# Optimization experiments

Measured on AMD Instinct MI355X. Metric: run time of the kernel, lower is better.

The kernel has to match this reference:

```python
import jax, jax.numpy as jnp
import numpy as np

ANG = 5   # angular resolution (u = v = 5, n = 25 views)
CH = 64   # input channels
D = 2 * CH  # spa_dim + ang_dim + fre_dim = c/2 + c/2 + c = 128
NEG = -1e15


def _l2(x):
    # torch F.normalize over the contraction axis (last axis of folded layout)
    n = jnp.sqrt(jnp.sum(x * x, axis=-1, keepdims=True))
    return x / jnp.maximum(n, 1e-12)


def setup_inputs() -> dict:
    key = jax.random.key(0)
    ks = jax.random.split(key, 8)
    b, c, n, h, w = 4, CH, ANG * ANG, 32, 32
    d = D
    return {
        "x_lf": jax.random.normal(ks[0], (b, c, n, h, w), jnp.float32),
        "x_hf": jax.random.normal(ks[1], (b, c, n, h, w), jnp.float32),
        "W_in": jax.random.normal(ks[2], (c, d), jnp.float32) / np.sqrt(c).astype(np.float32),
        "W_kv": jax.random.normal(ks[3], (c, d), jnp.float32) / np.sqrt(c).astype(np.float32),
        "ln_g": jnp.ones((d,), jnp.float32),
        "ln_b": jnp.zeros((d,), jnp.float32),
        "W_m1": jax.random.normal(ks[4], (d, d), jnp.float32) / np.sqrt(d).astype(np.float32),
        "W_m2": jax.random.normal(ks[5], (d, d), jnp.float32) / np.sqrt(d).astype(np.float32),
        "W_out": jax.random.normal(ks[6], (d, c), jnp.float32) / np.sqrt(d).astype(np.float32),
    }


def _attend(fold, unfold, tq, tk, tv):
    # fold(t): (b, cc, u*v, h, w) -> (b, M, K); k/v use the same folding
    qf = _l2(fold(tq))            # q normalized over contraction axis
    kf = _l2(fold(tk))            # k normalized over contraction axis (dim=-2 of k^T)
    vf = fold(tv)
    att = jnp.einsum('bmk,bnk->bmn', qf, kf)   # (b, M, M)
    M = att.shape[-1]
    tril = jnp.tril(jnp.ones((M, M), bool))    # causal mask over folded axis
    att = jax.nn.softmax(jnp.where(tril, att, NEG), axis=-1)
    return unfold(att @ vf) + tv               # residual with token_v


def reference(x_lf, x_hf, W_in, W_kv, ln_g, ln_b, W_m1, W_m2, W_out):
    b, c, n, h, w = x_hf.shape
    u = v = ANG
    d = W_in.shape[1]

    def to_tokens(x, W):
        # 'b c (u v) h w -> (b u v) (h w) c' ; Linear ; back to 'b d (u v) h w'
        xt = x.reshape(b, c, u, v, h, w).transpose(0, 2, 3, 4, 5, 1).reshape(b * u * v, h * w, c)
        y = xt @ W
        return y.reshape(b, u, v, h, w, d).transpose(0, 5, 1, 2, 3, 4).reshape(b, d, u * v, h, w)

    q = to_tokens(x_hf, W_in)
    kv = to_tokens(x_lf, W_kv)
    cq = d // 4
    sf_q, af_q, sa_q = q[:, :cq], q[:, cq:2 * cq], q[:, 2 * cq:]
    sf_kv, af_kv, sa_kv = kv[:, :cq], kv[:, cq:2 * cq], kv[:, 2 * cq:]

    # SpatialFrequency: 'b c (u v) h w -> b (c h) (w u v)'
    def sf_fold(t):
        cc = t.shape[1]
        return t.reshape(b, cc, u, v, h, w).transpose(0, 1, 4, 5, 2, 3).reshape(b, cc * h, w * u * v)
    def sf_unfold(t):
        cc = t.shape[1] // h
        return t.reshape(b, cc, h, w, u, v).transpose(0, 1, 4, 5, 2, 3).reshape(b, cc, u * v, h, w)

    # AngularFrequency: 'b c (u v) h w -> b (c u) (h v w)'
    def af_fold(t):
        cc = t.shape[1]
        return t.reshape(b, cc, u, v, h, w).transpose(0, 1, 2, 4, 3, 5).reshape(b, cc * u, h * v * w)
    def af_unfold(t):
        cc = t.shape[1] // u
        return t.reshape(b, cc, u, h, v, w).transpose(0, 1, 2, 4, 3, 5).reshape(b, cc, u * v, h, w)

    # SpatialAngular: 'b c (u v) h w -> b (h u) (c v w)'
    def sa_fold(t):
        cc = t.shape[1]
        return t.reshape(b, cc, u, v, h, w).transpose(0, 4, 2, 1, 3, 5).reshape(b, h * u, cc * v * w)
    def sa_unfold(t):
        cc = t.shape[2] // (v * w) if t.ndim == 3 else t.shape[1]
        t = t.reshape(b, h, u, cc, v, w)
        return t.transpose(0, 3, 2, 4, 1, 5).reshape(b, cc, u * v, h, w)

    sf = _attend(sf_fold, sf_unfold, sf_q, sf_kv, sf_kv)
    af = _attend(af_fold, af_unfold, af_q, af_kv, af_kv)
    sa = _attend(sa_fold, sa_unfold, sa_q, sa_kv, sa_kv)

    cat = jnp.concatenate([sf, af, sa], axis=1)  # (b, d, n, h, w)
    ct = cat.reshape(b, d, u, v, h, w).transpose(0, 2, 3, 4, 5, 1).reshape(b * u * v, h * w, d)

    # c_mlp: LayerNorm -> Linear -> ReLU -> Linear (dropout is identity in eval)
    mu = jnp.mean(ct, axis=-1, keepdims=True)
    var = jnp.mean(jnp.square(ct - mu), axis=-1, keepdims=True)
    ln = (ct - mu) / jnp.sqrt(var + 1e-5) * ln_g + ln_b
    mlp = jax.nn.relu(ln @ W_m1) @ W_m2
    out_t = (mlp + ct) @ W_out  # residual then output projection

    out = out_t.reshape(b, u, v, h, w, -1).transpose(0, 5, 1, 2, 3, 4).reshape(b, -1, u * v, h, w)
    return out
```

## Files before the change

kernel.cpp:

```cpp
#include <hip/hip_runtime.h>

#define NSP   25600
#define HWC   1024

typedef __attribute__((ext_vector_type(8))) short bf8;
typedef __attribute__((ext_vector_type(4))) float f4;
#define MFMA(a,b,c) __builtin_amdgcn_mfma_f32_16x16x32_bf16(a, b, c, 0, 0, 0)
typedef unsigned short u16;

__device__ __forceinline__ u16 f2b(float f) {
    union { float f; unsigned u; } v; v.f = f;
    unsigned r = v.u + 0x7fffu + ((v.u >> 16) & 1u);
    return (u16)(r >> 16);
}
__device__ __forceinline__ float b2f(u16 h) {
    union { unsigned u; float f; } v; v.u = ((unsigned)h) << 16;
    return v.f;
}

__device__ __forceinline__ long row_base(int att, int b, int m) {
    if (att == 0) { int cc = m >> 5, h = m & 31;   return ((long)(b*128 + cc))*NSP + h*32; }
    else if (att == 1) { int cc = m / 5, u = m - cc*5; return ((long)(b*128 + 32 + cc))*NSP + u*5120; }
    else { int h = m / 5, u = m - h*5;            return ((long)(b*128 + 64))*NSP + u*5120 + h*32; }
}
__device__ __forceinline__ long chunk_off(int att, int kc) {
    if (att == 0) return (long)kc * 1024;
    else if (att == 1) return (long)kc * 32;
    else { int cc = kc / 5, v = kc - cc*5; return (long)cc*NSP + v*1024; }
}

__global__ __launch_bounds__(256) void k_prep(
        const float* __restrict__ Wi, const float* __restrict__ Wk,
        const float* __restrict__ W1, const float* __restrict__ W2,
        const float* __restrict__ Wo, u16* __restrict__ wbt) {
    int e = blockIdx.x * 256 + threadIdx.x;
    const float* src; int base, K, N;
    if (e < 8192)       { src = Wi; base = 0;     K = 64;  N = 128; }
    else if (e < 16384) { src = Wk; base = 8192;  K = 64;  N = 128; }
    else if (e < 32768) { src = W1; base = 16384; K = 128; N = 128; }
    else if (e < 49152) { src = W2; base = 32768; K = 128; N = 128; }
    else                { src = Wo; base = 49152; K = 128; N = 64;  }
    int local = e - base, n = local / K, k = local - n * K;
    wbt[e] = f2b(src[k * N + n]);
}

__global__ __launch_bounds__(256) void k_prep2(
        const float* __restrict__ W2, const float* __restrict__ Wo,
        u16* __restrict__ w2o) {
    int e = blockIdx.x * 256 + threadIdx.x;
    int o = e >> 7, k = e & 127;
    float s = 0.f;
    for (int n = 0; n < 128; ++n) s += W2[k * 128 + n] * Wo[n * 64 + o];
    w2o[e] = f2b(s);
}

__global__ __launch_bounds__(256) void k_tokens(
        const float* __restrict__ x_hf, const float* __restrict__ x_lf,
        const u16* __restrict__ wbt,
        u16* __restrict__ qb, u16* __restrict__ kvb) {
    int s0 = blockIdx.x * 64, b = blockIdx.y, which = blockIdx.z;
    const float* x  = which ? x_lf : x_hf;
    const u16* Wb = wbt + (which ? 8192 : 0);
    u16* out = which ? kvb : qb;
    __shared__ u16 Axs[64 * 72];
    __shared__ u16 Wl [128 * 72];
    int tid = threadIdx.x;
    for (int g = tid; g < 1024; g += 256) {
        int d = g >> 3, c8 = (g & 7) * 8;
        *(bf8*)&Wl[d * 72 + c8] = *(const bf8*)(Wb + d * 64 + c8);
    }
    for (int g = tid; g < 1024; g += 256) {
        int s = g & 63, c4 = (g >> 6) * 4;
        long xb = ((long)(b * 64 + c4)) * NSP + s0 + s;
        ushort4 pk;
        pk.x = f2b(x[xb]);
        pk.y = f2b(x[xb + NSP]);
        pk.z = f2b(x[xb + 2 * NSP]);
        pk.w = f2b(x[xb + 3 * NSP]);
        *(ushort4*)&Axs[s * 72 + c4] = pk;
    }
    __syncthreads();
    int w = tid >> 6, l = tid & 63, quad = l >> 4, col = l & 15;
    f4 z = {0.f, 0.f, 0.f, 0.f};
    f4 acc[8]; for (int i = 0; i < 8; ++i) acc[i] = z;
#pragma unroll
    for (int kc = 0; kc < 2; ++kc) {
        bf8 a = *(bf8*)&Axs[(w * 16 + col) * 72 + kc * 32 + quad * 8];
#pragma unroll
        for (int nt = 0; nt < 8; ++nt) {
            bf8 bb = *(bf8*)&Wl[(nt * 16 + col) * 72 + kc * 32 + quad * 8];
            acc[nt] = MFMA(a, bb, acc[nt]);
        }
    }
#pragma unroll
    for (int nt = 0; nt < 8; ++nt) {
        int d = nt * 16 + col;
        long base = ((long)(b * 128 + d)) * NSP + s0 + w * 16 + quad * 4;
        ushort4 pk;
        pk.x = f2b(acc[nt][0]); pk.y = f2b(acc[nt][1]);
        pk.z = f2b(acc[nt][2]); pk.w = f2b(acc[nt][3]);
        *(ushort4*)(out + base) = pk;
    }
}

__global__ __launch_bounds__(256) void k_sgemm_all(
        const u16* __restrict__ qb, const u16* __restrict__ kvb,
        u16* __restrict__ vt0, u16* __restrict__ vt1, u16* __restrict__ vt2,
        float* __restrict__ nq, float* __restrict__ nk,
        u16* __restrict__ Sb, float* __restrict__ Spart) {
    __shared__ __align__(16) u16 lds[2 * 64 * 72];
    int x = blockIdx.x, b = blockIdx.y;
    int tid = threadIdx.x, w = tid >> 6, l = tid & 63, quad = l >> 4, col = l & 15;
    if (x < 136) {
        u16* Qs = lds;
        u16* Ks = lds + 64 * 72;
        int t = x, i = 0;
        while (t >= (i + 1) * (i + 2) / 2) ++i;
        int j = t - i * (i + 1) / 2;
        int mt = i * 64, nt = j * 64;
        int srow = tid >> 2, g = tid & 3;
        int mr = mt + srow, nr = nt + srow;
        long qrow = ((long)(b * 128 + (mr >> 5))) * NSP + (mr & 31) * 32;
        long krow = ((long)(b * 128 + (nr >> 5))) * NSP + (nr & 31) * 32;
        f4 z = {0.f, 0.f, 0.f, 0.f};
        f4 acc[4]; for (int q = 0; q < 4; ++q) acc[q] = z;
        for (int kc = 0; kc < 25; kc += 2) {
            long co = (long)kc * 1024;
            bool two = (kc + 1 < 25);
            *(bf8*)&Qs[srow * 72 + g * 8] = *(const bf8*)(qb + qrow + co + g * 8);
            *(bf8*)&Ks[srow * 72 + g * 8] = *(const bf8*)(kvb + krow + co + g * 8);
            if (two) {
                *(bf8*)&Qs[srow * 72 + 32 + g * 8] =
                    *(const bf8*)(qb + qrow + co + 1024 + g * 8);
                *(bf8*)&Ks[srow * 72 + 32 + g * 8] =
                    *(const bf8*)(kvb + krow + co + 1024 + g * 8);
            }
            __syncthreads();
            bf8 a0 = *(bf8*)&Qs[(w * 16 + col) * 72 + quad * 8];
#pragma unroll
            for (int t2 = 0; t2 < 4; ++t2) {
                bf8 bb = *(bf8*)&Ks[(t2 * 16 + col) * 72 + quad * 8];
                acc[t2] = MFMA(a0, bb, acc[t2]);
            }
            if (two) {
                bf8 a1 = *(bf8*)&Qs[(w * 16 + col) * 72 + 32 + quad * 8];
#pragma unroll
                for (int t2 = 0; t2 < 4; ++t2) {
                    bf8 bb = *(bf8*)&Ks[(t2 * 16 + col) * 72 + 32 + quad * 8];
                    acc[t2] = MFMA(a1, bb, acc[t2]);
                }
            }
            __syncthreads();
        }
#pragma unroll
        for (int t2 = 0; t2 < 4; ++t2)
#pragma unroll
            for (int r = 0; r < 4; ++r) {
                int m = mt + w * 16 + quad * 4 + r, n = nt + t2 * 16 + col;
                float v = (n <= m) ? acc[t2][r] : 0.f;
                Sb[((long)b * 1024 + m) * 1024 + n] = f2b(v);
            }
    } else if (x < 586) {
        float* fl = (float*)lds;
        int x2 = x - 136;
        int t = x2 % 15, y = x2 / 15;
        int att, split, nsplit; float* base;
        if (y < 10) { att = 1; split = y;      nsplit = 10; base = Spart; }
        else        { att = 2; split = y - 10; nsplit = 20; base = Spart + 614400; }
        int i = 0;
        while (t >= (i + 1) * (i + 2) / 2) ++i;
        int j = t - i * (i + 1) / 2;
        int mt = i * 32, nt = j * 32;
        long rm0 = row_base(att, b, mt + col),      rm1 = row_base(att, b, mt + 16 + col);
        long rn0 = row_base(att, b, nt + col),      rn1 = row_base(att, b, nt + 16 + col);
        int ko = quad * 8;
        f4 z = {0.f, 0.f, 0.f, 0.f};
        f4 a00 = z, a01 = z, a10 = z, a11 = z;
#pragma unroll
        for (int s = 0; s < 4; ++s) {
            int kc = split * 16 + w * 4 + s;
            long co = chunk_off(att, kc);
            bf8 qa0 = *(const bf8*)(qb + rm0 + co + ko);
            bf8 qa1 = *(const bf8*)(qb + rm1 + co + ko);
            bf8 kb0 = *(const bf8*)(kvb + rn0 + co + ko);
            bf8 kb1 = *(const bf8*)(kvb + rn1 + co + ko);
            a00 = MFMA(qa0, kb0, a00); a01 = MFMA(qa0, kb1, a01);
            a10 = MFMA(qa1, kb0, a10); a11 = MFMA(qa1, kb1, a11);
        }
        float* my = fl + w * 1024;
#pragma unroll
        for (int r = 0; r < 4; ++r) {
            my[(quad * 4 + r) * 32 + col]            = a00[r];
            my[(quad * 4 + r) * 32 + 16 + col]       = a01[r];
            my[(16 + quad * 4 + r) * 32 + col]       = a10[r];
            my[(16 + quad * 4 + r) * 32 + 16 + col]  = a11[r];
        }
        __syncthreads();
        float* dst = base + ((long)((b * 15 + t) * nsplit + split)) * 1024;
        for (int e = tid; e < 1024; e += 256)
            dst[e] = fl[e] + fl[1024 + e] + fl[2048 + e] + fl[3072 + e];
    } else if (x < 786) {
        u16* T = lds;
        int xv = x - 586;
        int kc = xv >> 3, pt = (xv & 7) * 128;
        long co = (long)kc * 1024;
#pragma unroll
        for (int i = 0; i < 4; ++i) {
            int idx = i * 256 + tid;
            int r = idx >> 3, fq = (idx & 7) * 4;
            ushort4 e = *(const ushort4*)(kvb + row_base(0, b, pt + r) + co + fq);
            *(ushort4*)&T[r * 36 + fq] = e;
        }
        __syncthreads();
#pragma unroll
        for (int i = 0; i < 4; ++i) {
            int idx = i * 256 + tid;
            int f = idx >> 5, p4 = (idx & 31) * 4;
            ushort4 pk;
            pk.x = T[(p4    ) * 36 + f];
            pk.y = T[(p4 + 1) * 36 + f];
            pk.z = T[(p4 + 2) * 36 + f];
            pk.w = T[(p4 + 3) * 36 + f];
            *(ushort4*)(vt0 + (((long)b * 25 + kc) * 32 + f) * 1024 + pt + p4) = pk;
        }
    } else if (x < 3186) {
        u16* T = lds;
        int att, kc, pt, KC; u16* vt;
        if (x < 1586) { int y = x - 786;  att = 1; kc = y / 5;  pt = (y - kc * 5) * 32;  KC = 160; vt = vt1; }
        else          { int y = x - 1586; att = 2; kc = y / 5;  pt = (y - kc * 5) * 32;  KC = 320; vt = vt2; }
        long co = chunk_off(att, kc);
        {
            int r = tid >> 3, fq = (tid & 7) * 4;
            ushort4 e = *(const ushort4*)(kvb + row_base(att, b, pt + r) + co + fq);
            *(ushort4*)&T[r * 36 + fq] = e;
        }
        __syncthreads();
        {
            int f = tid >> 3, p4 = (tid & 7) * 4;
            ushort4 pk;
            pk.x = T[(p4    ) * 36 + f];
            pk.y = T[(p4 + 1) * 36 + f];
            pk.z = T[(p4 + 2) * 36 + f];
            pk.w = T[(p4 + 3) * 36 + f];
            *(ushort4*)(vt + (((long)b * KC + kc) * 32 + f) * 160 + pt + p4) = pk;
        }
    } else {
        int x2 = x - 3186;
        int which = x2 >= 336;
        int g = which ? x2 - 336 : x2;
        int att, m0, KC;
        if (g < 256)      { att = 0; m0 = g * 4;         KC = 25;  }
        else if (g < 296) { att = 1; m0 = (g - 256) * 4; KC = 160; }
        else              { att = 2; m0 = (g - 296) * 4; KC = 320; }
        const u16* src = which ? kvb : qb;
        float* dst = which ? nk : nq;
        int ww = tid >> 6, lane = tid & 63;
        int m = m0 + ww;
        long base = row_base(att, b, m);
        int K = KC * 32;
        float s = 0.f;
        for (int k8 = lane * 8; k8 < K; k8 += 512) {
            bf8 v = *(const bf8*)(src + base + chunk_off(att, k8 >> 5) + (k8 & 31));
#pragma unroll
            for (int j = 0; j < 8; ++j) { float f = b2f(((u16*)&v)[j]); s += f * f; }
        }
        for (int o = 32; o >= 1; o >>= 1) s += __shfl_xor(s, o);
        if (lane == 0) {
            int off = (att == 0) ? b * 1024 + m
                                 : ((att == 1) ? 4096 : 4736) + b * 160 + m;
            dst[off] = 1.f / fmaxf(sqrtf(s), 1e-12f);
        }
    }
}

__global__ __launch_bounds__(256) void k_softmax_all(
        const u16* __restrict__ Sb, u16* __restrict__ Pb,
        const float* __restrict__ Spart, const float* __restrict__ nq,
        const float* __restrict__ nk, u16* __restrict__ Pb12) {
    int xb = blockIdx.x, b = blockIdx.y, tid = threadIdx.x;
    if (xb < 256) {
        int w = tid >> 6, lane = tid & 63;
        int m = xb * 4 + w;
        const u16* row = Sb + ((long)b * 1024 + m) * 1024;
        u16* pr = Pb + ((long)b * 1024 + m) * 1024;
        int e0 = lane * 16;
        float rq = nq[b * 1024 + m];
        const float* nkb = nk + b * 1024 + e0;
        float rk[16];
        *(float4*)&rk[0]  = *(const float4*)(nkb);
        *(float4*)&rk[4]  = *(const float4*)(nkb + 4);
        *(float4*)&rk[8]  = *(const float4*)(nkb + 8);
        *(float4*)&rk[12] = *(const float4*)(nkb + 12);
        bf8 x0 = *(const bf8*)(row + e0);
        bf8 x1 = *(const bf8*)(row + e0 + 8);
        float v[16];
#pragma unroll
        for (int j = 0; j < 8; ++j) {
            v[j]     = b2f(((u16*)&x0)[j]) * rq * rk[j];
            v[8 + j] = b2f(((u16*)&x1)[j]) * rq * rk[8 + j];
        }
        float mx = -1e30f;
#pragma unroll
        for (int j = 0; j < 16; ++j) if (e0 + j <= m) mx = fmaxf(mx, v[j]);
#pragma unroll
        for (int o = 32; o >= 1; o >>= 1) mx = fmaxf(mx, __shfl_xor(mx, o));
        float s = 0.f;
#pragma unroll
        for (int j = 0; j < 16; ++j) {
            float e = (e0 + j <= m) ? __expf(v[j] - mx) : 0.f;
            v[j] = e; s += e;
        }
#pragma unroll
        for (int o = 32; o >= 1; o >>= 1) s += __shfl_xor(s, o);
        float inv = 1.f / s;
        bf8 o0, o1;
#pragma unroll
        for (int j = 0; j < 8; ++j) {
            ((u16*)&o0)[j] = f2b(v[j] * inv);
            ((u16*)&o1)[j] = f2b(v[8 + j] * inv);
        }
        *(bf8*)(pr + e0) = o0;
        *(bf8*)(pr + e0 + 8) = o1;
    } else {
        int x = xb - 256;
        int att = (x < 160) ? 1 : 2;
        int m = (att == 1) ? x : x - 160;
        int nsplit = (att == 1) ? 10 : 20;
        const float* base = (att == 1) ? Spart : Spart + 614400;
        int noff = (att == 1) ? 4096 : 4736;
        u16* P = Pb12 + ((att == 1) ? 0 : 102400);
        int i = m >> 5, ro = (m & 31) * 32;
        int n = tid;
        bool act = (n <= m) && (n < 160);
        float myv = 0.f;
        if (act) {
            int t = i * (i + 1) / 2 + (n >> 5);
            const float* src = base + ((long)((b * 15 + t) * nsplit)) * 1024 + ro + (n & 31);
            float s = 0.f;
            for (int sp = 0; sp < nsplit; ++sp) s += src[(long)sp * 1024];
            myv = s * (nq[noff + b * 160 + m] * nk[noff + b * 160 + n]);
        }
        __shared__ float red[256];
        red[tid] = act ? myv : -1e30f; __syncthreads();
        for (int w = 128; w >= 1; w >>= 1) {
            if (tid < w) red[tid] = fmaxf(red[tid], red[tid + w]);
            __syncthreads();
        }
        float mx = red[0]; __syncthreads();
        float e = act ? __expf(myv - mx) : 0.f;
        red[tid] = e; __syncthreads();
        for (int w = 128; w >= 1; w >>= 1) {
            if (tid < w) red[tid] += red[tid + w];
            __syncthreads();
        }
        float inv = 1.f / red[0];
        if (n < 160) P[((long)b * 160 + m) * 160 + n] = f2b(e * inv);
    }
}

__global__ __launch_bounds__(256) void k_ogemm_all(
        const u16* __restrict__ Pb, const u16* __restrict__ vt0,
        const u16* __restrict__ Pb12, const u16* __restrict__ vt1,
        const u16* __restrict__ vt2, const u16* __restrict__ kvb,
        u16* __restrict__ catb) {
    __shared__ __align__(16) u16 lds[64 * 72 + 32 * 72];
    int x = blockIdx.x, b = blockIdx.y;
    int tid = threadIdx.x, w = tid >> 6, l = tid & 63, quad = l >> 4, col = l & 15;
    if (x < 400) {
        int mtt = x & 15, kc = x >> 4;
        int mt = mtt * 64;
        long co = (long)kc * 1024;
        const u16* vtc = vt0 + ((long)b * 25 + kc) * 32 * 1024;
        u16* Ps = lds;
        u16* Vs = lds + 64 * 72;
        f4 z = {0.f, 0.f, 0.f, 0.f};
        f4 acc[2]; acc[0] = z; acc[1] = z;
        for (int s = 0; s <= mtt; ++s) {
            int p0 = s * 64;
#pragma unroll
            for (int i = 0; i < 2; ++i) {
                int idx = i * 256 + tid;
                int row = idx >> 3, c8 = (idx & 7) * 8;
                *(bf8*)&Ps[row * 72 + c8] =
                    *(const bf8*)(Pb + ((long)(b * 1024 + mt + row)) * 1024 + p0 + c8);
            }
            {
                int f = tid >> 3, p8 = (tid & 7) * 8;
                *(bf8*)&Vs[f * 72 + p8] =
                    *(const bf8*)(vtc + (long)f * 1024 + p0 + p8);
            }
            __syncthreads();
            bf8 a0 = *(bf8*)&Ps[(w * 16 + col) * 72 + quad * 8];
            bf8 a1 = *(bf8*)&Ps[(w * 16 + col) * 72 + 32 + quad * 8];
#pragma unroll
            for (int t2 = 0; t2 < 2; ++t2) {
                bf8 b0 = *(bf8*)&Vs[(t2 * 16 + col) * 72 + quad * 8];
                bf8 b1 = *(bf8*)&Vs[(t2 * 16 + col) * 72 + 32 + quad * 8];
                acc[t2] = MFMA(a0, b0, acc[t2]);
                acc[t2] = MFMA(a1, b1, acc[t2]);
            }
            __syncthreads();
        }
#pragma unroll
        for (int t2 = 0; t2 < 2; ++t2)
#pragma unroll
            for (int r = 0; r < 4; ++r) {
                int m = mt + w * 16 + quad * 4 + r, f = t2 * 16 + col;
                long adr = ((long)(b * 128 + (m >> 5))) * NSP + (m & 31) * 32 + co + f;
                catb[adr] = f2b(acc[t2][r] + b2f(kvb[adr]));
            }
    } else {
        int x2 = x - 400;
        int att = (x2 < 320) ? 1 : 2;
        int ft  = (att == 1) ? x2 : x2 - 320;
        int KC  = (att == 1) ? 160 : 320;
        const u16* vt = (att == 1) ? vt1 : vt2;
        const u16* Prow = Pb12 + ((att == 1) ? 0 : 102400) + (long)b * 160 * 160;
        u16* Vs = lds;
        for (int g = tid; g < 320; g += 256) {
            int fl = g / 20, p8 = (g % 20) * 8;
            int fglob = ft * 16 + fl;
            int kc = fglob >> 5, fr = fglob & 31;
            *(bf8*)&Vs[fl * 168 + p8] =
                *(const bf8*)(vt + (((long)b * KC + kc) * 32 + fr) * 160 + p8);
        }
        __syncthreads();
        int fglob = ft * 16 + col;
        int kcf = fglob >> 5, fi = fglob & 31;
        long cbase = chunk_off(att, kcf) + fi;
        f4 z = {0.f, 0.f, 0.f, 0.f};
        for (int j = 0; j < 3; ++j) {
            int mi = w + 4 * j;
            if (mi >= 10) break;
            int nkk = (mi >> 1) + 1;
            f4 acc = z;
#pragma unroll 5
            for (int kk = 0; kk < nkk; ++kk) {
                bf8 a  = *(const bf8*)(Prow + (mi * 16 + col) * 160 + kk * 32 + quad * 8);
                bf8 bb = *(bf8*)&Vs[col * 168 + kk * 32 + quad * 8];
                acc = MFMA(a, bb, acc);
            }
#pragma unroll
            for (int r = 0; r < 4; ++r) {
                int m = mi * 16 + quad * 4 + r;
                long adr = row_base(att, b, m) + cbase;
                catb[adr] = f2b(acc[r] + b2f(kvb[adr]));
            }
        }
    }
}

__global__ __launch_bounds__(256) void k_mlp_fused(
        const u16* __restrict__ catb, const float* __restrict__ g,
        const float* __restrict__ be, const u16* __restrict__ wbt,
        const u16* __restrict__ w2o, float* __restrict__ out) {
    int x = blockIdx.x, tid = threadIdx.x;
    int tt = x * 64;
    int bn = tt >> 10, hwt = tt & 1023;
    int b = bn / 25, uv = bn - b * 25;
    __shared__ u16 CT[64 * 136];
    __shared__ u16 Wt[128 * 136];
    __shared__ float gl[128], bl[128], mu_s[64], rs_s[64];
    int w = tid >> 6, l = tid & 63, quad = l >> 4, col = l & 15;
    const u16* src = catb + (long)b * 128 * NSP + (long)uv * HWC + hwt;
#pragma unroll
    for (int i = 0; i < 4; ++i) {
        int gi = i * 256 + tid;
        int d = gi >> 3, hw8 = (gi & 7) * 8;
        bf8 v = *(const bf8*)(src + (long)d * NSP + hw8);
#pragma unroll
        for (int j = 0; j < 8; ++j) CT[(hw8 + j) * 136 + d] = ((u16*)&v)[j];
    }
    {
        const u16* Wob = wbt + 49152;
        for (int q = tid; q < 1024; q += 256) {
            int o = q >> 4, k8 = (q & 15) * 8;
            *(bf8*)&Wt[o * 136 + k8] = *(const bf8*)(Wob + o * 128 + k8);
        }
    }
    if (tid < 128) { gl[tid] = g[tid]; bl[tid] = be[tid]; }
    __syncthreads();
    f4 z = {0.f, 0.f, 0.f, 0.f};
    f4 acc_o[4]; for (int i = 0; i < 4; ++i) acc_o[i] = z;
#pragma unroll
    for (int kc = 0; kc < 4; ++kc) {
        bf8 a = *(bf8*)&CT[(w * 16 + col) * 136 + kc * 32 + quad * 8];
#pragma unroll
        for (int nt = 0; nt < 4; ++nt) {
            bf8 bb = *(bf8*)&Wt[(nt * 16 + col) * 136 + kc * 32 + quad * 8];
            acc_o[nt] = MFMA(a, bb, acc_o[nt]);
        }
    }
    {
        int tk = w * 16 + (l >> 2), dg = (l & 3) * 32;
        float s = 0.f, s2 = 0.f;
#pragma unroll
        for (int q = 0; q < 4; ++q) {
            bf8 vv = *(bf8*)&CT[tk * 136 + dg + q * 8];
#pragma unroll
            for (int j = 0; j < 8; ++j) { float f = b2f(((u16*)&vv)[j]); s += f; s2 += f * f; }
        }
        s += __shfl_xor(s, 1); s2 += __shfl_xor(s2, 1);
        s += __shfl_xor(s, 2); s2 += __shfl_xor(s2, 2);
        if ((l & 3) == 0) {
            float m = s * (1.f / 128.f);
            float var = s2 * (1.f / 128.f) - m * m;
            mu_s[tk] = m; rs_s[tk] = rsqrtf(var + 1e-5f);
        }
    }
    __syncthreads();
    for (int q = tid; q < 1024; q += 256) {
        int row = q >> 4, k8 = (q & 15) * 8;
        bf8 cv = *(bf8*)&CT[row * 136 + k8];
        float m = mu_s[row], rs = rs_s[row];
        bf8 av;
#pragma unroll
        for (int j = 0; j < 8; ++j)
            ((u16*)&av)[j] = f2b((b2f(((u16*)&cv)[j]) - m) * rs * gl[k8 + j] + bl[k8 + j]);
        *(bf8*)&CT[row * 136 + k8] = av;
    }
    {
        const u16* W1b = wbt + 16384;
        for (int q = tid; q < 2048; q += 256) {
            int n = q >> 4, k8 = (q & 15) * 8;
            *(bf8*)&Wt[n * 136 + k8] = *(const bf8*)(W1b + n * 128 + k8);
        }
    }
    __syncthreads();
    f4 acc_h[8]; for (int i = 0; i < 8; ++i) acc_h[i] = z;
#pragma unroll
    for (int kc = 0; kc < 4; ++kc) {
        bf8 a = *(bf8*)&CT[(w * 16 + col) * 136 + kc * 32 + quad * 8];
#pragma unroll
        for (int nt = 0; nt < 8; ++nt) {
            bf8 bb = *(bf8*)&Wt[(nt * 16 + col) * 136 + kc * 32 + quad * 8];
            acc_h[nt] = MFMA(a, bb, acc_h[nt]);
        }
    }
    __syncthreads();
#pragma unroll
    for (int nt = 0; nt < 8; ++nt)
#pragma unroll
        for (int r = 0; r < 4; ++r) {
            int row = w * 16 + quad * 4 + r, n = nt * 16 + col;
            CT[row * 136 + n] = f2b(fmaxf(acc_h[nt][r], 0.f));
        }
    for (int q = tid; q < 1024; q += 256) {
        int o = q >> 4, k8 = (q & 15) * 8;
        *(bf8*)&Wt[o * 136 + k8] = *(const bf8*)(w2o + o * 128 + k8);
    }
    __syncthreads();
#pragma unroll
    for (int kc = 0; kc < 4; ++kc) {
        bf8 a = *(bf8*)&CT[(w * 16 + col) * 136 + kc * 32 + quad * 8];
#pragma unroll
        for (int nt = 0; nt < 4; ++nt) {
            bf8 bb = *(bf8*)&Wt[(nt * 16 + col) * 136 + kc * 32 + quad * 8];
            acc_o[nt] = MFMA(a, bb, acc_o[nt]);
        }
    }
    int hw = hwt + w * 16 + quad * 4;
#pragma unroll
    for (int nt = 0; nt < 4; ++nt) {
        int o = nt * 16 + col;
        float4 pk = {acc_o[nt][0], acc_o[nt][1], acc_o[nt][2], acc_o[nt][3]};
        *(float4*)(out + ((long)((b * 64 + o) * 25 + uv)) * 1024 + hw) = pk;
    }
}

extern "C" void kernel_launch(void* const* d_in, const int* in_sizes, int n_in,
                              void* d_out, int out_size, void* d_ws, size_t ws_size,
                              hipStream_t stream) {
    const float* x_lf = (const float*)d_in[0];
    const float* x_hf = (const float*)d_in[1];
    const float* W_in = (const float*)d_in[2];
    const float* W_kv = (const float*)d_in[3];
    const float* ln_g = (const float*)d_in[4];
    const float* ln_b = (const float*)d_in[5];
    const float* W_m1 = (const float*)d_in[6];
    const float* W_m2 = (const float*)d_in[7];
    const float* W_ot = (const float*)d_in[8];
    float* out = (float*)d_out;

    float* ws = (float*)d_ws;
    u16*   qb    = (u16*)ws;
    u16*   kvb   = (u16*)(ws + 6553600);
    u16*   catb  = (u16*)(ws + 13107200);
    u16*   Sb    = (u16*)(ws + 26214400);
    u16*   Pb    = (u16*)(ws + 28311552);
    u16*   Pb12  = (u16*)(ws + 30408704);
    float* Spart = ws + 30511104;
    float* nq    = ws + 32354304;
    float* nk    = ws + 32359680;
    u16*   w2ob  = (u16*)(ws + 32365056);
    u16*   vt0   = (u16*)(ws + 32569856);
    u16*   vt1   = (u16*)(ws + 34208256);
    u16*   vt2   = (u16*)(ws + 35846656);
    u16*   wbt   = (u16*)(ws + 39123456);

    k_prep<<<dim3(224), 256, 0, stream>>>(W_in, W_kv, W_m1, W_m2, W_ot, wbt);
    k_prep2<<<dim3(32), 256, 0, stream>>>(W_m2, W_ot, w2ob);

    k_tokens<<<dim3(400, 4, 2), 256, 0, stream>>>(x_hf, x_lf, wbt, qb, kvb);

    k_sgemm_all<<<dim3(3858, 4), 256, 0, stream>>>(qb, kvb, vt0, vt1, vt2,
                                                   nq, nk, Sb, Spart);

    k_softmax_all<<<dim3(576, 4), 256, 0, stream>>>(Sb, Pb, Spart, nq, nk, Pb12);

    k_ogemm_all<<<dim3(1360, 4), 256, 0, stream>>>(Pb, vt0, Pb12, vt1, vt2, kvb, catb);

    k_mlp_fused<<<dim3(1600), 256, 0, stream>>>(catb, ln_g, ln_b, wbt, w2ob, out);
}
```

Before: 267.1 us.

## Widen SF output GEMM tiles, coarsen V-transpose blocks, merge weight prep kernels

The spatial-frequency output GEMM now has each block compute up to 64 feature columns (two K-chunks) instead of 32. This lets the causal P tile loaded into LDS be reused across four MFMA column tiles rather than two, and heavy (large mtt) blocks are scheduled first. The att1/att2 V-transpose blocks now process all 160 rows of a chunk per block instead of 32, which cuts the block count of the sgemm launch. The two weight-prep kernels are merged into one launch. The trade-offs are fewer, heavier blocks with more accumulators and LDS per block, so fewer blocks can be resident per CU.

```diff
diff --git a/kernel.cpp b/kernel.cpp
--- a/kernel.cpp
+++ b/kernel.cpp
@@ -32,26 +32,26 @@
 __global__ __launch_bounds__(256) void k_prep(
         const float* __restrict__ Wi, const float* __restrict__ Wk,
         const float* __restrict__ W1, const float* __restrict__ W2,
-        const float* __restrict__ Wo, u16* __restrict__ wbt) {
-    int e = blockIdx.x * 256 + threadIdx.x;
-    const float* src; int base, K, N;
-    if (e < 8192)       { src = Wi; base = 0;     K = 64;  N = 128; }
-    else if (e < 16384) { src = Wk; base = 8192;  K = 64;  N = 128; }
-    else if (e < 32768) { src = W1; base = 16384; K = 128; N = 128; }
-    else if (e < 49152) { src = W2; base = 32768; K = 128; N = 128; }
-    else                { src = Wo; base = 49152; K = 128; N = 64;  }
-    int local = e - base, n = local / K, k = local - n * K;
-    wbt[e] = f2b(src[k * N + n]);
-}
-
-__global__ __launch_bounds__(256) void k_prep2(
-        const float* __restrict__ W2, const float* __restrict__ Wo,
+        const float* __restrict__ Wo, u16* __restrict__ wbt,
         u16* __restrict__ w2o) {
-    int e = blockIdx.x * 256 + threadIdx.x;
-    int o = e >> 7, k = e & 127;
-    float s = 0.f;
-    for (int n = 0; n < 128; ++n) s += W2[k * 128 + n] * Wo[n * 64 + o];
-    w2o[e] = f2b(s);
+    int x = blockIdx.x, tid = threadIdx.x;
+    if (x < 224) {
+        int e = x * 256 + tid;
+        const float* src; int base, K, N;
+        if (e < 8192)       { src = Wi; base = 0;     K = 64;  N = 128; }
+        else if (e < 16384) { src = Wk; base = 8192;  K = 64;  N = 128; }
+        else if (e < 32768) { src = W1; base = 16384; K = 128; N = 128; }
+        else if (e < 49152) { src = W2; base = 32768; K = 128; N = 128; }
+        else                { src = Wo; base = 49152; K = 128; N = 64;  }
+        int local = e - base, n = local / K, k = local - n * K;
+        wbt[e] = f2b(src[k * N + n]);
+    } else {
+        int e = (x - 224) * 256 + tid;
+        int o = e >> 7, k = e & 127;
+        float s = 0.f;
+        for (int n = 0; n < 128; ++n) s += W2[k * 128 + n] * Wo[n * 64 + o];
+        w2o[e] = f2b(s);
+    }
 }
 
 __global__ __launch_bounds__(256) void k_tokens(
@@ -223,29 +223,29 @@
             pk.w = T[(p4 + 3) * 36 + f];
             *(ushort4*)(vt0 + (((long)b * 25 + kc) * 32 + f) * 1024 + pt + p4) = pk;
         }
-    } else if (x < 3186) {
+    } else if (x < 1266) {
         u16* T = lds;
-        int att, kc, pt, KC; u16* vt;
-        if (x < 1586) { int y = x - 786;  att = 1; kc = y / 5;  pt = (y - kc * 5) * 32;  KC = 160; vt = vt1; }
-        else          { int y = x - 1586; att = 2; kc = y / 5;  pt = (y - kc * 5) * 32;  KC = 320; vt = vt2; }
+        int att, kc, KC; u16* vt;
+        if (x < 946) { att = 1; kc = x - 786; KC = 160; vt = vt1; }
+        else         { att = 2; kc = x - 946; KC = 320; vt = vt2; }
         long co = chunk_off(att, kc);
-        {
-            int r = tid >> 3, fq = (tid & 7) * 4;
-            ushort4 e = *(const ushort4*)(kvb + row_base(att, b, pt + r) + co + fq);
+        for (int g = tid; g < 1280; g += 256) {
+            int r = g >> 3, fq = (g & 7) * 4;
+            ushort4 e = *(const ushort4*)(kvb + row_base(att, b, r) + co + fq);
             *(ushort4*)&T[r * 36 + fq] = e;
         }
         __syncthreads();
-        {
-            int f = tid >> 3, p4 = (tid & 7) * 4;
+        for (int g = tid; g < 1280; g += 256) {
+            int f = g / 40, p4 = (g % 40) * 4;
             ushort4 pk;
             pk.x = T[(p4    ) * 36 + f];
             pk.y = T[(p4 + 1) * 36 + f];
             pk.z = T[(p4 + 2) * 36 + f];
             pk.w = T[(p4 + 3) * 36 + f];
-            *(ushort4*)(vt + (((long)b * KC + kc) * 32 + f) * 160 + pt + p4) = pk;
+            *(ushort4*)(vt + (((long)b * KC + kc) * 32 + f) * 160 + p4) = pk;
         }
     } else {
-        int x2 = x - 3186;
+        int x2 = x - 1266;
         int which = x2 >= 336;
         int g = which ? x2 - 336 : x2;
         int att, m0, KC;
@@ -363,18 +363,19 @@
         const u16* __restrict__ Pb12, const u16* __restrict__ vt1,
         const u16* __restrict__ vt2, const u16* __restrict__ kvb,
         u16* __restrict__ catb) {
-    __shared__ __align__(16) u16 lds[64 * 72 + 32 * 72];
+    __shared__ __align__(16) u16 lds[64 * 72 + 64 * 72];
     int x = blockIdx.x, b = blockIdx.y;
     int tid = threadIdx.x, w = tid >> 6, l = tid & 63, quad = l >> 4, col = l & 15;
-    if (x < 400) {
-        int mtt = x & 15, kc = x >> 4;
+    if (x < 208) {
+        int fg = x % 13, mtt = 15 - x / 13;
         int mt = mtt * 64;
-        long co = (long)kc * 1024;
-        const u16* vtc = vt0 + ((long)b * 25 + kc) * 32 * 1024;
+        int nf = (fg == 12) ? 2 : 4;
         u16* Ps = lds;
         u16* Vs = lds + 64 * 72;
         f4 z = {0.f, 0.f, 0.f, 0.f};
-        f4 acc[2]; acc[0] = z; acc[1] = z;
+        f4 acc[4];
+#pragma unroll
+        for (int i = 0; i < 4; ++i) acc[i] = z;
         for (int s = 0; s <= mtt; ++s) {
             int p0 = s * 64;
 #pragma unroll
@@ -384,16 +385,22 @@
                 *(bf8*)&Ps[row * 72 + c8] =
                     *(const bf8*)(Pb + ((long)(b * 1024 + mt + row)) * 1024 + p0 + c8);
             }
-            {
-                int f = tid >> 3, p8 = (tid & 7) * 8;
-                *(bf8*)&Vs[f * 72 + p8] =
-                    *(const bf8*)(vtc + (long)f * 1024 + p0 + p8);
+#pragma unroll
+            for (int i = 0; i < 2; ++i) {
+                int idx = i * 256 + tid;
+                int f = idx >> 3, p8 = (idx & 7) * 8;
+                if (f < nf * 16) {
+                    int kc = fg * 2 + (f >> 5), fr = f & 31;
+                    *(bf8*)&Vs[f * 72 + p8] =
+                        *(const bf8*)(vt0 + (((long)(b * 25 + kc)) * 32 + fr) * 1024 + p0 + p8);
+                }
             }
             __syncthreads();
             bf8 a0 = *(bf8*)&Ps[(w * 16 + col) * 72 + quad * 8];
             bf8 a1 = *(bf8*)&Ps[(w * 16 + col) * 72 + 32 + quad * 8];
 #pragma unroll
-            for (int t2 = 0; t2 < 2; ++t2) {
+            for (int t2 = 0; t2 < 4; ++t2) {
+                if (t2 >= nf) break;
                 bf8 b0 = *(bf8*)&Vs[(t2 * 16 + col) * 72 + quad * 8];
                 bf8 b1 = *(bf8*)&Vs[(t2 * 16 + col) * 72 + 32 + quad * 8];
                 acc[t2] = MFMA(a0, b0, acc[t2]);
@@ -402,15 +409,20 @@
             __syncthreads();
         }
 #pragma unroll
-        for (int t2 = 0; t2 < 2; ++t2)
+        for (int t2 = 0; t2 < 4; ++t2) {
+            if (t2 >= nf) break;
+            int fglob = fg * 64 + t2 * 16 + col;
+            int kc = fglob >> 5, fi = fglob & 31;
 #pragma unroll
             for (int r = 0; r < 4; ++r) {
-                int m = mt + w * 16 + quad * 4 + r, f = t2 * 16 + col;
-                long adr = ((long)(b * 128 + (m >> 5))) * NSP + (m & 31) * 32 + co + f;
+                int m = mt + w * 16 + quad * 4 + r;
+                long adr = ((long)(b * 128 + (m >> 5))) * NSP + (m & 31) * 32
+                         + (long)kc * 1024 + fi;
                 catb[adr] = f2b(acc[t2][r] + b2f(kvb[adr]));
             }
+        }
     } else {
-        int x2 = x - 400;
+        int x2 = x - 208;
         int att = (x2 < 320) ? 1 : 2;
         int ft  = (att == 1) ? x2 : x2 - 320;
         int KC  = (att == 1) ? 160 : 320;
@@ -598,17 +610,16 @@
     u16*   vt2   = (u16*)(ws + 35846656);
     u16*   wbt   = (u16*)(ws + 39123456);
 
-    k_prep<<<dim3(224), 256, 0, stream>>>(W_in, W_kv, W_m1, W_m2, W_ot, wbt);
-    k_prep2<<<dim3(32), 256, 0, stream>>>(W_m2, W_ot, w2ob);
+    k_prep<<<dim3(256), 256, 0, stream>>>(W_in, W_kv, W_m1, W_m2, W_ot, wbt, w2ob);
 
     k_tokens<<<dim3(400, 4, 2), 256, 0, stream>>>(x_hf, x_lf, wbt, qb, kvb);
 
-    k_sgemm_all<<<dim3(3858, 4), 256, 0, stream>>>(qb, kvb, vt0, vt1, vt2,
+    k_sgemm_all<<<dim3(1938, 4), 256, 0, stream>>>(qb, kvb, vt0, vt1, vt2,
                                                    nq, nk, Sb, Spart);
 
     k_softmax_all<<<dim3(576, 4), 256, 0, stream>>>(Sb, Pb, Spart, nq, nk, Pb12);
 
-    k_ogemm_all<<<dim3(1360, 4), 256, 0, stream>>>(Pb, vt0, Pb12, vt1, vt2, kvb, catb);
+    k_ogemm_all<<<dim3(1168, 4), 256, 0, stream>>>(Pb, vt0, Pb12, vt1, vt2, kvb, catb);
 
     k_mlp_fused<<<dim3(1600), 256, 0, stream>>>(catb, ln_g, ln_b, wbt, w2ob, out);
 }
```

New measurement: 266.4 us. About the same (-0.3%).
